# Performance work log

Measured on AMD Instinct MI355X. Metric: run time of the kernel, lower is better.

The kernel has to match this reference:

```python
import jax, jax.numpy as jnp
import numpy as np
import math

N = 8192
D_IN = 1024
D_H = 1024

def setup_inputs() -> dict:
    key = jax.random.key(0)
    k_h, k_q, k_k, k_v = jax.random.split(key, 4)
    s = 1.0 / math.sqrt(D_IN)
    return {
        "h": jax.random.normal(k_h, (N, D_IN), dtype=jnp.float32),
        "wq": jax.random.uniform(k_q, (D_H, D_IN), dtype=jnp.float32, minval=-s, maxval=s),
        "wk": jax.random.uniform(k_k, (D_H, D_IN), dtype=jnp.float32, minval=-s, maxval=s),
        "wv": jax.random.uniform(k_v, (D_H, D_IN), dtype=jnp.float32, minval=-s, maxval=s),
    }

def reference(h, wq, wk, wv):
    # nn.Linear with no bias: x @ W.T
    q = h @ wq.T  # [N, D_H]
    k = h @ wk.T  # [N, D_H]
    v = h @ wv.T  # [N, D_H]
    scale = 1.0 / math.sqrt(q.shape[-1])
    z = (q @ k.T) * scale          # [N, N]
    beta = jax.nn.softmax(z, axis=1)
    return beta @ v                 # [N, D_H]
```

## Files before the change

### kernel.cpp

```cpp
#include <hip/hip_runtime.h>
#include <hip/hip_bf16.h>
#include <stdint.h>
#include <math.h>

typedef __bf16 bf16;
typedef __bf16 bf16x8 __attribute__((ext_vector_type(8)));
typedef __bf16 bf16x4 __attribute__((ext_vector_type(4)));
typedef float  f32x4  __attribute__((ext_vector_type(4)));
typedef int    i32x4  __attribute__((ext_vector_type(4)));
typedef int    i32x16 __attribute__((ext_vector_type(16)));

#define AS_GLOBAL __attribute__((address_space(1)))
#define AS_LDS    __attribute__((address_space(3)))

__device__ __forceinline__ void gload_lds16(const void* g, void* l) {
    __builtin_amdgcn_global_load_lds((const AS_GLOBAL uint32_t*)g,
                                     (AS_LDS uint32_t*)l, 16, 0, 0);
}
__device__ __forceinline__ void cfence() { asm volatile("" ::: "memory"); }
#define BAR()    do { cfence(); __builtin_amdgcn_s_barrier(); cfence(); } while (0)
#define WAITV(n) asm volatile("s_waitcnt vmcnt(" #n ")" ::: "memory")
#define WAITL0() asm volatile("s_waitcnt lgkmcnt(0)" ::: "memory")

#define QSC 36.0f
#define QDQ (1.0f / (QSC * QSC * 32.0f))

__device__ __forceinline__ int qi8(float f) {
    int q = (int)rintf(f);
    return q > 127 ? 127 : (q < -127 ? -127 : q);
}

__global__ __launch_bounds__(256) void cvt_f32_to_bf16(const float* __restrict__ in,
                                                       bf16* __restrict__ out, int n4) {
    int i = blockIdx.x * 256 + threadIdx.x;
    if (i >= n4) return;
    const float4* p = (const float4*)in;
    float4 v = p[i];
    bf16x4 o;
    o[0] = (bf16)v.x; o[1] = (bf16)v.y; o[2] = (bf16)v.z; o[3] = (bf16)v.w;
    *(bf16x4*)(out + (size_t)i * 4) = o;
}

__global__ __launch_bounds__(256) void cvt_qk_i8(const bf16* __restrict__ QKV,
                                                 int8_t* __restrict__ Qi8,
                                                 int8_t* __restrict__ Ki8) {
    int i = blockIdx.x * 256 + threadIdx.x;
    int base = i * 8;
    int row = base >> 11;
    int c = base & 2047;
    bf16x8 v = *(const bf16x8*)(QKV + (size_t)row * 3072 + c);
    uint32_t w0 = 0, w1 = 0;
    #pragma unroll
    for (int j = 0; j < 4; ++j) w0 |= (uint32_t)(qi8((float)v[j] * QSC) & 0xff) << (8 * j);
    #pragma unroll
    for (int j = 0; j < 4; ++j) w1 |= (uint32_t)(qi8((float)v[j + 4] * QSC) & 0xff) << (8 * j);
    int8_t* dst = (c < 1024) ? (Qi8 + (size_t)row * 1024 + c)
                             : (Ki8 + (size_t)row * 1024 + (c - 1024));
    uint2 pk; pk.x = w0; pk.y = w1;
    *(uint2*)dst = pk;
}

__global__ __launch_bounds__(512, 2) void gemmEi8(const int8_t* __restrict__ A,
                                                  const int8_t* __restrict__ B,
                                                  bf16* __restrict__ E,
                                                  int K, int ld, int ldc, int nbn) {
    __shared__ char smem[131072];

    const int tid  = threadIdx.x;
    const int lane = tid & 63;
    const int wave = tid >> 6;
    const int wr   = wave >> 2;
    const int wc   = wave & 3;

    const int cpx = gridDim.x >> 3;
    const int swz = ((int)blockIdx.x & 7) * cpx + ((int)blockIdx.x >> 3);
    const int bm = swz / nbn, bn = swz % nbn;
    const int NT = K >> 7;

    const int r0 = tid >> 3;
    const int c0 = ((tid & 7) ^ (r0 & 7)) << 4;
    const int8_t* Abase = A + (size_t)(bm * 256 + r0) * ld + c0;
    const int8_t* Bbase = B + (size_t)(bn * 256 + r0) * ld + c0;

    auto stA = [&](int t, int h) {
        char* d = smem + ((t & 1) << 15) + (h << 14) + (tid << 4);
        gload_lds16(Abase + ((size_t)(h * 128)     ) * ld + t * 128, d);
        gload_lds16(Abase + ((size_t)(h * 128) + 64) * ld + t * 128, d + 8192);
    };
    auto stB = [&](int t, int h) {
        char* d = smem + 65536 + ((t & 1) << 15) + (h << 14) + (tid << 4);
        gload_lds16(Bbase + ((size_t)(h * 128)     ) * ld + t * 128, d);
        gload_lds16(Bbase + ((size_t)(h * 128) + 64) * ld + t * 128, d + 8192);
    };
    auto rdFrag = [&](const char* hbase, int rr, int kk) -> i32x4 {
        int slot = ((kk << 1) + (lane >> 5)) ^ (rr & 7);
        return *(const i32x4*)(hbase + rr * 128 + (slot << 4));
    };
    auto rdA = [&](int t, int m, int kk) -> i32x4 {
        const char* hb = smem + ((t & 1) << 15) + (wr << 14);
        return rdFrag(hb, m * 32 + (lane & 31), kk);
    };
    auto rdB = [&](int t, int n, int kk) -> i32x4 {
        int gr = wc * 64 + n * 32 + (lane & 31);
        const char* hb = smem + 65536 + ((t & 1) << 15) + ((gr >> 7) << 14);
        return rdFrag(hb, gr & 127, kk);
    };

    i32x16 acc[4][2] = {};
    i32x4 a[4][4], b[2][4];

#define MM16(MO) \
    _Pragma("unroll") for (int m_ = 0; m_ < 2; ++m_) \
    _Pragma("unroll") for (int n_ = 0; n_ < 2; ++n_) \
    _Pragma("unroll") for (int k_ = 0; k_ < 4; ++k_) \
        acc[m_ + MO][n_] = __builtin_amdgcn_mfma_i32_32x32x32_i8( \
            a[m_ + MO][k_], b[n_][k_], acc[m_ + MO][n_], 0, 0, 0);

    stA(0, 0); stA(0, 1); stB(0, 0); stB(0, 1);
    stA(1, 0); stA(1, 1); stB(1, 0);
    WAITV(6);
    BAR();

    for (int t = 0; t < NT; ++t) {
        if (t + 1 < NT) stB(t + 1, 1);
        #pragma unroll
        for (int m_ = 0; m_ < 4; ++m_)
            #pragma unroll
            for (int k_ = 0; k_ < 4; ++k_) a[m_][k_] = rdA(t, m_, k_);
        #pragma unroll
        for (int n_ = 0; n_ < 2; ++n_)
            #pragma unroll
            for (int k_ = 0; k_ < 4; ++k_) b[n_][k_] = rdB(t, n_, k_);
        __builtin_amdgcn_s_setprio(1);
        MM16(0);
        __builtin_amdgcn_s_setprio(0);
        WAITL0();
        BAR();
        if (t + 2 < NT) { stA(t + 2, 0); stA(t + 2, 1); stB(t + 2, 0); }
        __builtin_amdgcn_s_setprio(1);
        MM16(2);
        __builtin_amdgcn_s_setprio(0);
        if (t + 2 < NT)      { WAITV(6); }
        else if (t + 1 < NT) { WAITV(0); }
        BAR();
    }
#undef MM16

    const int crow0 = bm * 256 + wr * 128 + 4 * (lane >> 5);
    const int ccol0 = bn * 256 + wc * 64 + (lane & 31);
    #pragma unroll
    for (int mi = 0; mi < 4; ++mi)
        #pragma unroll
        for (int ni = 0; ni < 2; ++ni)
            #pragma unroll
            for (int r = 0; r < 16; ++r) {
                int row = crow0 + mi * 32 + (r & 3) + 8 * (r >> 2);
                E[(size_t)row * ldc + ccol0 + ni * 32] =
                    (bf16)__expf((float)acc[mi][ni][r] * QDQ);
            }
}

template<typename CT, int BN, int SPLIT>
__global__ __launch_bounds__(512, 2) void gemmW(const bf16* __restrict__ A,
                                                const bf16* __restrict__ B,
                                                CT* __restrict__ C,
                                                CT* __restrict__ C2,
                                                int K, int lda, int ldb, int ldc,
                                                int nbn) {
    constexpr int NBH = BN / 128;
    constexpr int NR  = BN / 64;
    constexpr int NHF = NR / 2;
    __shared__ char smem[65536 + NBH * 32768];

    const int tid  = threadIdx.x;
    const int lane = tid & 63;
    const int wave = tid >> 6;
    const int wr   = wave >> 2;
    const int wc   = wave & 3;
    const int frow = lane & 15;
    const int fg   = lane >> 4;

    const int cpx = gridDim.x >> 3;
    const int swz = ((int)blockIdx.x & 7) * cpx + ((int)blockIdx.x >> 3);
    int id = swz, s = 0;
    if (SPLIT == 2) { s = id & 1; id >>= 1; }
    const int bm = id / nbn, bn = id % nbn;
    const int NT = K >> 6;
    const size_t koff = (size_t)s * K;
    CT* Cp = (SPLIT == 2 && s == 1) ? C2 : C;

    const int r0 = tid >> 3;
    const int c0 = ((tid & 7) ^ (r0 & 7)) << 3;
    const bf16* Abase = A + (size_t)(bm * 256 + r0) * lda + c0 + koff;
    const bf16* Bbase = B + (size_t)(bn * BN + r0) * ldb + c0 + koff;

    auto stA = [&](int t, int h) {
        char* d = smem + ((t & 1) << 15) + (h << 14) + (tid << 4);
        gload_lds16(Abase + ((size_t)(h * 128)      ) * lda + t * 64, d);
        gload_lds16(Abase + ((size_t)(h * 128) + 64 ) * lda + t * 64, d + 8192);
    };
    auto stB = [&](int t, int h) {
        char* d = smem + 65536 + (t & 1) * (NBH * 16384) + (h << 14) + (tid << 4);
        gload_lds16(Bbase + ((size_t)(h * 128)      ) * ldb + t * 64, d);
        gload_lds16(Bbase + ((size_t)(h * 128) + 64 ) * ldb + t * 64, d + 8192);
    };
    auto rdA = [&](int t, int m, int kk) -> bf16x8 {
        int r = m * 16 + frow;
        return *(const bf16x8*)(smem + ((t & 1) << 15) + (wr << 14)
                + r * 128 + ((((kk << 2) + fg) ^ (frow & 7)) << 4));
    };
    auto rdB = [&](int t, int n, int kk) -> bf16x8 {
        int br = wc * (BN / 4) + n * 16 + frow;
        return *(const bf16x8*)(smem + 65536 + (t & 1) * (NBH * 16384) + ((br >> 7) << 14)
                + (br & 127) * 128 + ((((kk << 2) + fg) ^ (frow & 7)) << 4));
    };

    f32x4 acc[8][NR] = {};
    bf16x8 aLo[4][2], aHi[4][2], bLo[NHF][2], bHi[NHF][2];

#define MMQ(MO, NO, AARR, BARR) \
    _Pragma("unroll") for (int m_ = 0; m_ < 4; ++m_) \
    _Pragma("unroll") for (int n_ = 0; n_ < NHF; ++n_) \
    _Pragma("unroll") for (int k_ = 0; k_ < 2; ++k_) \
        acc[m_ + MO][n_ + NO] = __builtin_amdgcn_mfma_f32_16x16x32_bf16( \
            AARR[m_][k_], BARR[n_][k_], acc[m_ + MO][n_ + NO], 0, 0, 0);

    stA(0, 0); stA(0, 1);
    stB(0, 0); if constexpr (NBH == 2) stB(0, 1);
    stA(1, 0); stA(1, 1);
    if constexpr (NBH == 2) { stB(1, 0); WAITV(6); } else { WAITV(4); }
    BAR();

    for (int t = 0; t < NT; ++t) {
        if (t + 1 < NT) stB(t + 1, NBH - 1);
        #pragma unroll
        for (int m_ = 0; m_ < 4; ++m_) { aLo[m_][0] = rdA(t, m_, 0); aLo[m_][1] = rdA(t, m_, 1); }
        #pragma unroll
        for (int n_ = 0; n_ < NHF; ++n_) { bLo[n_][0] = rdB(t, n_, 0); bLo[n_][1] = rdB(t, n_, 1); }
        #pragma unroll
        for (int n_ = 0; n_ < NHF; ++n_) { bHi[n_][0] = rdB(t, NHF + n_, 0); bHi[n_][1] = rdB(t, NHF + n_, 1); }
        #pragma unroll
        for (int m_ = 0; m_ < 4; ++m_) { aHi[m_][0] = rdA(t, 4 + m_, 0); aHi[m_][1] = rdA(t, 4 + m_, 1); }
        __builtin_amdgcn_s_setprio(1);
        MMQ(0, 0, aLo, bLo);
        MMQ(0, NHF, aLo, bHi);
        __builtin_amdgcn_s_setprio(0);
        WAITL0();
        BAR();
        if (t + 2 < NT) {
            stA(t + 2, 0); stA(t + 2, 1);
            if constexpr (NBH == 2) stB(t + 2, 0);
        }
        __builtin_amdgcn_s_setprio(1);
        MMQ(4, NHF, aHi, bHi);
        MMQ(4, 0, aHi, bLo);
        __builtin_amdgcn_s_setprio(0);
        if (t + 2 < NT) {
            if constexpr (NBH == 2) WAITV(6); else WAITV(4);
        } else if (t + 1 < NT) {
            WAITV(0);
        }
        BAR();
    }
#undef MMQ

    const size_t crow0 = (size_t)bm * 256 + wr * 128 + (fg << 2);
    const size_t ccol0 = (size_t)bn * BN + wc * (BN / 4) + frow;
    #pragma unroll
    for (int m = 0; m < 8; ++m)
        #pragma unroll
        for (int n = 0; n < NR; ++n)
            #pragma unroll
            for (int i = 0; i < 4; ++i)
                Cp[(crow0 + m * 16 + i) * ldc + ccol0 + n * 16] = (CT)(acc[m][n][i]);
}

__global__ __launch_bounds__(256) void rowsum_inv(const bf16* __restrict__ E,
                                                  float* __restrict__ inv, int cols) {
    __shared__ float red[4];
    const int tid = threadIdx.x;
    const bf16* er = E + (size_t)blockIdx.x * cols;
    float s = 0.f;
    #pragma unroll
    for (int it = 0; it < 4; ++it) {
        bf16x8 v = *(const bf16x8*)(er + it * 2048 + tid * 8);
        #pragma unroll
        for (int j = 0; j < 8; ++j) s += (float)v[j];
    }
    #pragma unroll
    for (int o = 32; o; o >>= 1) s += __shfl_xor(s, o);
    if ((tid & 63) == 0) red[tid >> 6] = s;
    __syncthreads();
    if (tid == 0) inv[blockIdx.x] = 1.0f / (red[0] + red[1] + red[2] + red[3]);
}

__global__ __launch_bounds__(256) void add_scale(float* __restrict__ out,
                                                 const float* __restrict__ part,
                                                 const float* __restrict__ inv, int n4) {
    int i = blockIdx.x * 256 + threadIdx.x;
    if (i >= n4) return;
    const float sc = inv[i >> 8];
    float4 a = ((const float4*)out)[i];
    float4 b = ((const float4*)part)[i];
    a.x = (a.x + b.x) * sc; a.y = (a.y + b.y) * sc;
    a.z = (a.z + b.z) * sc; a.w = (a.w + b.w) * sc;
    ((float4*)out)[i] = a;
}

__global__ __launch_bounds__(256) void transpose_bf16(const ushort* __restrict__ V,
                                                      ushort* __restrict__ VT,
                                                      int R, int ld) {
    __shared__ ushort tile[32][33];
    const int tx = threadIdx.x, ty = threadIdx.y;
    const int r0 = blockIdx.y * 32, c0 = blockIdx.x * 32;
    #pragma unroll
    for (int i = 0; i < 32; i += 8)
        tile[ty + i][tx] = V[(size_t)(r0 + ty + i) * ld + c0 + tx];
    __syncthreads();
    #pragma unroll
    for (int i = 0; i < 32; i += 8)
        VT[(size_t)(c0 + ty + i) * R + r0 + tx] = tile[tx][ty + i];
}

extern "C" void kernel_launch(void* const* d_in, const int* in_sizes, int n_in,
                              void* d_out, int out_size, void* d_ws, size_t ws_size,
                              hipStream_t stream) {
    const float* h  = (const float*)d_in[0];
    const float* wq = (const float*)d_in[1];
    const float* wk = (const float*)d_in[2];
    const float* wv = (const float*)d_in[3];
    float* out = (float*)d_out;

    char* ws = (char*)d_ws;
    bf16*   h_bf = (bf16*)(ws);
    bf16*   wcat = (bf16*)(ws + (16ull << 20));
    bf16*   QKV  = (bf16*)(ws + (22ull << 20));
    bf16*   VT   = (bf16*)(ws + (70ull << 20));
    bf16*   E    = (bf16*)(ws + (86ull << 20));
    int8_t* Qi8  = (int8_t*)(ws);
    int8_t* Ki8  = (int8_t*)(ws + (8ull << 20));
    float*  Pv   = (float*)(ws);
    float*  invp = (float*)(ws + (33ull << 20));

    cvt_f32_to_bf16<<<8192, 256, 0, stream>>>(h,  h_bf, (8192 * 1024) / 4);
    cvt_f32_to_bf16<<<1024, 256, 0, stream>>>(wq, wcat,               (1024 * 1024) / 4);
    cvt_f32_to_bf16<<<1024, 256, 0, stream>>>(wk, wcat + 1024 * 1024, (1024 * 1024) / 4);
    cvt_f32_to_bf16<<<1024, 256, 0, stream>>>(wv, wcat + 2048 * 1024, (1024 * 1024) / 4);

    gemmW<bf16, 256, 1><<<384, 512, 0, stream>>>(h_bf, wcat, QKV, nullptr,
                                                 1024, 1024, 1024, 3072, 12);

    cvt_qk_i8<<<8192, 256, 0, stream>>>(QKV, Qi8, Ki8);

    transpose_bf16<<<dim3(32, 256), dim3(32, 8), 0, stream>>>(
        (const ushort*)(QKV + 2048), (ushort*)VT, 8192, 3072);

    gemmEi8<<<1024, 512, 0, stream>>>(Qi8, Ki8, E, 1024, 1024, 8192, 32);

    rowsum_inv<<<8192, 256, 0, stream>>>(E, invp, 8192);

    gemmW<float, 256, 2><<<256, 512, 0, stream>>>(E, VT, out, Pv,
                                                  4096, 8192, 8192, 1024, 4);

    add_scale<<<8192, 256, 0, stream>>>(out, Pv, invp, (8192 * 1024) / 4);
}
```

Measured before the change: 344.9 us.

## Fuse softmax row sums into QK epilogue and add 32x32 MFMA PV kernel

Row sums of exp(scores) are now computed inside the QK^T int8 GEMM epilogue with shuffle reductions and atomicAdd into a zeroed buffer. This removes the separate rowsum pass that re-read the 128MB E matrix. The PV GEMM moves to a dedicated kernel using 32x32x16 bf16 MFMA with a different LDS fragment layout, replacing the 16x16 gemmW instance. The price is atomics and a per-row-dependent summation order, plus a small zeroing kernel.

Result: slower. 470.1 us (+36.3%).

```diff
diff --git a/kernel.cpp b/kernel.cpp
--- a/kernel.cpp
+++ b/kernel.cpp
@@ -7,6 +7,7 @@
 typedef __bf16 bf16x8 __attribute__((ext_vector_type(8)));
 typedef __bf16 bf16x4 __attribute__((ext_vector_type(4)));
 typedef float  f32x4  __attribute__((ext_vector_type(4)));
+typedef float  f32x16 __attribute__((ext_vector_type(16)));
 typedef int    i32x4  __attribute__((ext_vector_type(4)));
 typedef int    i32x16 __attribute__((ext_vector_type(16)));
 
@@ -41,6 +42,11 @@
     *(bf16x4*)(out + (size_t)i * 4) = o;
 }
 
+__global__ __launch_bounds__(256) void zero_f32(float* __restrict__ p, int n) {
+    int i = blockIdx.x * 256 + threadIdx.x;
+    if (i < n) p[i] = 0.f;
+}
+
 __global__ __launch_bounds__(256) void cvt_qk_i8(const bf16* __restrict__ QKV,
                                                  int8_t* __restrict__ Qi8,
                                                  int8_t* __restrict__ Ki8) {
@@ -63,6 +69,7 @@
 __global__ __launch_bounds__(512, 2) void gemmEi8(const int8_t* __restrict__ A,
                                                   const int8_t* __restrict__ B,
                                                   bf16* __restrict__ E,
+                                                  float* __restrict__ sums,
                                                   int K, int ld, int ldc, int nbn) {
     __shared__ char smem[131072];
 
@@ -149,22 +156,142 @@
     const int crow0 = bm * 256 + wr * 128 + 4 * (lane >> 5);
     const int ccol0 = bn * 256 + wc * 64 + (lane & 31);
     #pragma unroll
-    for (int mi = 0; mi < 4; ++mi)
-        #pragma unroll
-        for (int ni = 0; ni < 2; ++ni)
+    for (int mi = 0; mi < 4; ++mi) {
+        float rs[16];
+        #pragma unroll
+        for (int r = 0; r < 16; ++r) {
+            int row = crow0 + mi * 32 + (r & 3) + 8 * (r >> 2);
+            float e0 = __expf((float)acc[mi][0][r] * QDQ);
+            float e1 = __expf((float)acc[mi][1][r] * QDQ);
+            bf16 b0 = (bf16)e0, b1 = (bf16)e1;
+            E[(size_t)row * ldc + ccol0]      = b0;
+            E[(size_t)row * ldc + ccol0 + 32] = b1;
+            rs[r] = (float)b0 + (float)b1;
+        }
+        #pragma unroll
+        for (int r = 0; r < 16; ++r)
+            #pragma unroll
+            for (int off = 1; off <= 16; off <<= 1)
+                rs[r] += __shfl_xor(rs[r], off);
+        if ((lane & 31) == 0) {
             #pragma unroll
             for (int r = 0; r < 16; ++r) {
                 int row = crow0 + mi * 32 + (r & 3) + 8 * (r >> 2);
-                E[(size_t)row * ldc + ccol0 + ni * 32] =
-                    (bf16)__expf((float)acc[mi][ni][r] * QDQ);
+                atomicAdd(&sums[row], rs[r]);
             }
-}
-
-template<typename CT, int BN, int SPLIT>
+        }
+    }
+}
+
+__global__ __launch_bounds__(512, 2) void gemmPV(const bf16* __restrict__ A,
+                                                 const bf16* __restrict__ B,
+                                                 float* __restrict__ C,
+                                                 float* __restrict__ C2,
+                                                 int K, int lda, int ldb, int ldc,
+                                                 int nbn) {
+    __shared__ char smem[131072];
+
+    const int tid  = threadIdx.x;
+    const int lane = tid & 63;
+    const int wave = tid >> 6;
+    const int wr   = wave >> 2;
+    const int wc   = wave & 3;
+
+    const int cpx = gridDim.x >> 3;
+    const int swz = ((int)blockIdx.x & 7) * cpx + ((int)blockIdx.x >> 3);
+    int id = swz;
+    const int s = id & 1; id >>= 1;
+    const int bm = id / nbn, bn = id % nbn;
+    const int NT = K >> 6;
+    const size_t koff = (size_t)s * K;
+    float* Cp = (s == 1) ? C2 : C;
+
+    const int r0 = tid >> 3;
+    const int c0 = ((tid & 7) ^ (r0 & 7)) << 3;
+    const bf16* Abase = A + (size_t)(bm * 256 + r0) * lda + c0 + koff;
+    const bf16* Bbase = B + (size_t)(bn * 256 + r0) * ldb + c0 + koff;
+
+    auto stA = [&](int t, int h) {
+        char* d = smem + ((t & 1) << 15) + (h << 14) + (tid << 4);
+        gload_lds16(Abase + ((size_t)(h * 128)     ) * lda + t * 64, d);
+        gload_lds16(Abase + ((size_t)(h * 128) + 64) * lda + t * 64, d + 8192);
+    };
+    auto stB = [&](int t, int h) {
+        char* d = smem + 65536 + ((t & 1) << 15) + (h << 14) + (tid << 4);
+        gload_lds16(Bbase + ((size_t)(h * 128)     ) * ldb + t * 64, d);
+        gload_lds16(Bbase + ((size_t)(h * 128) + 64) * ldb + t * 64, d + 8192);
+    };
+    auto rdFrag = [&](const char* hbase, int rr, int kk) -> bf16x8 {
+        int slot = ((kk << 1) + (lane >> 5)) ^ (rr & 7);
+        return *(const bf16x8*)(hbase + rr * 128 + (slot << 4));
+    };
+    auto rdA = [&](int t, int m, int kk) -> bf16x8 {
+        const char* hb = smem + ((t & 1) << 15) + (wr << 14);
+        return rdFrag(hb, m * 32 + (lane & 31), kk);
+    };
+    auto rdB = [&](int t, int n, int kk) -> bf16x8 {
+        int gr = wc * 64 + n * 32 + (lane & 31);
+        const char* hb = smem + 65536 + ((t & 1) << 15) + ((gr >> 7) << 14);
+        return rdFrag(hb, gr & 127, kk);
+    };
+
+    f32x16 acc[4][2] = {};
+    bf16x8 a[4][4], b[2][4];
+
+#define MM16B(MO) \
+    _Pragma("unroll") for (int m_ = 0; m_ < 2; ++m_) \
+    _Pragma("unroll") for (int n_ = 0; n_ < 2; ++n_) \
+    _Pragma("unroll") for (int k_ = 0; k_ < 4; ++k_) \
+        acc[m_ + MO][n_] = __builtin_amdgcn_mfma_f32_32x32x16_bf16( \
+            a[m_ + MO][k_], b[n_][k_], acc[m_ + MO][n_], 0, 0, 0);
+
+    stA(0, 0); stA(0, 1); stB(0, 0); stB(0, 1);
+    stA(1, 0); stA(1, 1); stB(1, 0);
+    WAITV(6);
+    BAR();
+
+    for (int t = 0; t < NT; ++t) {
+        if (t + 1 < NT) stB(t + 1, 1);
+        #pragma unroll
+        for (int m_ = 0; m_ < 4; ++m_)
+            #pragma unroll
+            for (int k_ = 0; k_ < 4; ++k_) a[m_][k_] = rdA(t, m_, k_);
+        #pragma unroll
+        for (int n_ = 0; n_ < 2; ++n_)
+            #pragma unroll
+            for (int k_ = 0; k_ < 4; ++k_) b[n_][k_] = rdB(t, n_, k_);
+        __builtin_amdgcn_s_setprio(1);
+        MM16B(0);
+        __builtin_amdgcn_s_setprio(0);
+        WAITL0();
+        BAR();
+        if (t + 2 < NT) { stA(t + 2, 0); stA(t + 2, 1); stB(t + 2, 0); }
+        __builtin_amdgcn_s_setprio(1);
+        MM16B(2);
+        __builtin_amdgcn_s_setprio(0);
+        if (t + 2 < NT)      { WAITV(6); }
+        else if (t + 1 < NT) { WAITV(0); }
+        BAR();
+    }
+#undef MM16B
+
+    const int crow0 = bm * 256 + wr * 128 + 4 * (lane >> 5);
+    const int ccol0 = bn * 256 + wc * 64 + (lane & 31);
+    #pragma unroll
+    for (int mi = 0; mi < 4; ++mi)
+        #pragma unroll
+        for (int ni = 0; ni < 2; ++ni)
+            #pragma unroll
+            for (int r = 0; r < 16; ++r) {
+                int row = crow0 + mi * 32 + (r & 3) + 8 * (r >> 2);
+                Cp[(size_t)row * ldc + ccol0 + ni * 32] = acc[mi][ni][r];
+            }
+}
+
+template<typename CT, int BN>
 __global__ __launch_bounds__(512, 2) void gemmW(const bf16* __restrict__ A,
                                                 const bf16* __restrict__ B,
                                                 CT* __restrict__ C,
-                                                CT* __restrict__ C2,
                                                 int K, int lda, int ldb, int ldc,
                                                 int nbn) {
     constexpr int NBH = BN / 128;
@@ -182,17 +309,13 @@
 
     const int cpx = gridDim.x >> 3;
     const int swz = ((int)blockIdx.x & 7) * cpx + ((int)blockIdx.x >> 3);
-    int id = swz, s = 0;
-    if (SPLIT == 2) { s = id & 1; id >>= 1; }
-    const int bm = id / nbn, bn = id % nbn;
+    const int bm = swz / nbn, bn = swz % nbn;
     const int NT = K >> 6;
-    const size_t koff = (size_t)s * K;
-    CT* Cp = (SPLIT == 2 && s == 1) ? C2 : C;
 
     const int r0 = tid >> 3;
     const int c0 = ((tid & 7) ^ (r0 & 7)) << 3;
-    const bf16* Abase = A + (size_t)(bm * 256 + r0) * lda + c0 + koff;
-    const bf16* Bbase = B + (size_t)(bn * BN + r0) * ldb + c0 + koff;
+    const bf16* Abase = A + (size_t)(bm * 256 + r0) * lda + c0;
+    const bf16* Bbase = B + (size_t)(bn * BN + r0) * ldb + c0;
 
     auto stA = [&](int t, int h) {
         char* d = smem + ((t & 1) << 15) + (h << 14) + (tid << 4);
@@ -272,34 +395,15 @@
         for (int n = 0; n < NR; ++n)
             #pragma unroll
             for (int i = 0; i < 4; ++i)
-                Cp[(crow0 + m * 16 + i) * ldc + ccol0 + n * 16] = (CT)(acc[m][n][i]);
-}
-
-__global__ __launch_bounds__(256) void rowsum_inv(const bf16* __restrict__ E,
-                                                  float* __restrict__ inv, int cols) {
-    __shared__ float red[4];
-    const int tid = threadIdx.x;
-    const bf16* er = E + (size_t)blockIdx.x * cols;
-    float s = 0.f;
-    #pragma unroll
-    for (int it = 0; it < 4; ++it) {
-        bf16x8 v = *(const bf16x8*)(er + it * 2048 + tid * 8);
-        #pragma unroll
-        for (int j = 0; j < 8; ++j) s += (float)v[j];
-    }
-    #pragma unroll
-    for (int o = 32; o; o >>= 1) s += __shfl_xor(s, o);
-    if ((tid & 63) == 0) red[tid >> 6] = s;
-    __syncthreads();
-    if (tid == 0) inv[blockIdx.x] = 1.0f / (red[0] + red[1] + red[2] + red[3]);
+                C[(crow0 + m * 16 + i) * ldc + ccol0 + n * 16] = (CT)(acc[m][n][i]);
 }
 
 __global__ __launch_bounds__(256) void add_scale(float* __restrict__ out,
                                                  const float* __restrict__ part,
-                                                 const float* __restrict__ inv, int n4) {
+                                                 const float* __restrict__ sums, int n4) {
     int i = blockIdx.x * 256 + threadIdx.x;
     if (i >= n4) return;
-    const float sc = inv[i >> 8];
+    const float sc = 1.0f / sums[i >> 8];
     float4 a = ((const float4*)out)[i];
     float4 b = ((const float4*)part)[i];
     a.x = (a.x + b.x) * sc; a.y = (a.y + b.y) * sc;
@@ -340,27 +444,27 @@
     int8_t* Qi8  = (int8_t*)(ws);
     int8_t* Ki8  = (int8_t*)(ws + (8ull << 20));
     float*  Pv   = (float*)(ws);
-    float*  invp = (float*)(ws + (33ull << 20));
+    float*  sums = (float*)(ws + (33ull << 20));
 
     cvt_f32_to_bf16<<<8192, 256, 0, stream>>>(h,  h_bf, (8192 * 1024) / 4);
     cvt_f32_to_bf16<<<1024, 256, 0, stream>>>(wq, wcat,               (1024 * 1024) / 4);
     cvt_f32_to_bf16<<<1024, 256, 0, stream>>>(wk, wcat + 1024 * 1024, (1024 * 1024) / 4);
     cvt_f32_to_bf16<<<1024, 256, 0, stream>>>(wv, wcat + 2048 * 1024, (1024 * 1024) / 4);
 
-    gemmW<bf16, 256, 1><<<384, 512, 0, stream>>>(h_bf, wcat, QKV, nullptr,
-                                                 1024, 1024, 1024, 3072, 12);
+    gemmW<bf16, 256><<<384, 512, 0, stream>>>(h_bf, wcat, QKV,
+                                              1024, 1024, 1024, 3072, 12);
 
     cvt_qk_i8<<<8192, 256, 0, stream>>>(QKV, Qi8, Ki8);
 
     transpose_bf16<<<dim3(32, 256), dim3(32, 8), 0, stream>>>(
         (const ushort*)(QKV + 2048), (ushort*)VT, 8192, 3072);
 
-    gemmEi8<<<1024, 512, 0, stream>>>(Qi8, Ki8, E, 1024, 1024, 8192, 32);
-
-    rowsum_inv<<<8192, 256, 0, stream>>>(E, invp, 8192);
-
-    gemmW<float, 256, 2><<<256, 512, 0, stream>>>(E, VT, out, Pv,
-                                                  4096, 8192, 8192, 1024, 4);
-
-    add_scale<<<8192, 256, 0, stream>>>(out, Pv, invp, (8192 * 1024) / 4);
-}
+    zero_f32<<<32, 256, 0, stream>>>(sums, 8192);
+
+    gemmEi8<<<1024, 512, 0, stream>>>(Qi8, Ki8, E, sums, 1024, 1024, 8192, 32);
+
+    gemmPV<<<256, 512, 0, stream>>>(E, VT, out, Pv,
+                                    4096, 8192, 8192, 1024, 4);
+
+    add_scale<<<8192, 256, 0, stream>>>(out, Pv, sums, (8192 * 1024) / 4);
+}
```
